# Kernel optimization log

Measured on AMD Instinct MI355X. Metric: run time of the kernel, lower is better.

Reference implementation:

```python
import jax, jax.numpy as jnp
import numpy as np

N = 20000   # nodes
E = 320000  # edges
G = 64      # graphs in batch
IN = 256    # in_dim
H = 256     # hidden_dim1
C = 2       # n_classes


def setup_inputs() -> dict:
    key = jax.random.key(0)
    ks = jax.random.split(key, 12)
    h = jax.random.normal(ks[0], (N, IN), jnp.float32)
    src = jax.random.randint(ks[1], (E,), 0, N)
    dst = jax.random.randint(ks[2], (E,), 0, N)
    graph_id = jnp.sort(jax.random.randint(ks[3], (N,), 0, G))
    s_in = 1.0 / np.sqrt(IN)
    s_h = 1.0 / np.sqrt(H)
    W_conv = jax.random.normal(ks[4], (IN, H), jnp.float32) * s_in
    b_conv = jnp.zeros((H,), jnp.float32)
    w_gate = jax.random.normal(ks[5], (H, 1), jnp.float32) * s_h
    b_gate = jnp.zeros((1,), jnp.float32)
    W1 = jax.random.normal(ks[6], (H, H), jnp.float32) * s_h
    b1 = jnp.zeros((H,), jnp.float32)
    W2 = jax.random.normal(ks[7], (H, C), jnp.float32) * s_h
    b2 = jnp.zeros((C,), jnp.float32)
    return dict(h=h, src=src, dst=dst, graph_id=graph_id, W_conv=W_conv,
                b_conv=b_conv, w_gate=w_gate, b_gate=b_gate, W1=W1, b1=b1,
                W2=W2, b2=b2)


def reference(h, src, dst, graph_id, W_conv, b_conv, w_gate, b_gate, W1, b1, W2, b2):
    ones_e = jnp.ones((E,), jnp.float32)
    # DGL GraphConv, norm='both': D_out^-1/2 on source, D_in^-1/2 on dest
    deg_out = jax.ops.segment_sum(ones_e, src, num_segments=N)
    deg_in = jax.ops.segment_sum(ones_e, dst, num_segments=N)
    hn = h * jax.lax.rsqrt(jnp.maximum(deg_out, 1.0))[:, None]
    hn = hn @ W_conv                       # [N, H] (weight applied before aggregation)
    agg = jax.ops.segment_sum(hn[src], dst, num_segments=N)  # gather + scatter-add
    agg = agg * jax.lax.rsqrt(jnp.maximum(deg_in, 1.0))[:, None] + b_conv
    hr = jax.nn.relu(agg)                  # F.relu after conv1
    # GlobalAttentionPooling: per-graph segment softmax over gate scores
    gate = hr @ w_gate + b_gate            # [N, 1]
    gmax = jax.ops.segment_max(gate, graph_id, num_segments=G)
    e = jnp.exp(gate - gmax[graph_id])
    denom = jax.ops.segment_sum(e, graph_id, num_segments=G)
    att = e / denom[graph_id]              # [N, 1] attention weights (g2)
    hg = jax.ops.segment_sum(att * hr, graph_id, num_segments=G)  # [G, H]
    # classifier heads (dropout is identity at inference)
    a2 = hg @ W1 + b1
    a3 = a2 @ W2 + b2
    return jax.nn.sigmoid(a3), att, hg
```

## Files before the change

### kernel.cpp

```cpp
#include <hip/hip_runtime.h>
#include <hip/hip_bf16.h>
#include <hip/hip_fp16.h>
#include <math.h>

#define NN 20000
#define EE 320000
#define GG 64
#define IND 256
#define HD 256
#define CC 2

typedef __hip_bfloat16 bf16;
typedef __attribute__((ext_vector_type(8))) short short8;
typedef __attribute__((ext_vector_type(4))) float f32x4;

__device__ __forceinline__ float b2f(bf16 x){ return __bfloat162float(x); }
__device__ __forceinline__ float bits2f(unsigned short b){
    union{ float f; unsigned u; } v; v.u = ((unsigned)b) << 16; return v.f;
}
__device__ __forceinline__ short f2bs(float x){
    union{ bf16 b; short s; } u; u.b = __float2bfloat16(x); return u.s;
}
__device__ __forceinline__ float ldf3(const void* p, size_t i, int c){
    if (c == 1) return b2f(((const bf16*)p)[i]);
    if (c == 2) return __half2float(((const __half*)p)[i]);
    return ((const float*)p)[i];
}
__device__ __forceinline__ int idec(const void* p, int i, int c){
    if (c == 1) return (int)(((const long long*)p)[i]);
    if (c == 2) return (int)(((const float*)p)[i]);
    if (c == 3) return (int)__half2float(((const __half*)p)[i]);
    return ((const int*)p)[i];
}

__global__ void k_detect(const void* src, const void* dst, const void* gid,
                         const unsigned short* h, const unsigned short* Wc,
                         const unsigned short* wg, const unsigned short* W1,
                         const unsigned short* W2, const unsigned short* bc,
                         int* icode, int* dcode){
    int blk = blockIdx.x;
    if (blk < 3){
        if (threadIdx.x != 0) return;
        const void* buf = (blk == 0) ? src : (blk == 1) ? dst : gid;
        int n     = (blk == 2) ? NN : EE;
        int bound = (blk == 2) ? GG : NN;
        int ok64 = 1, ok32 = 1, okf32 = 1, okf16 = 1;
        const long long* p64 = (const long long*)buf;
        for (int i = 0; i < 64; i++){
            long long v = p64[n/8 + i];
            if (v < 0 || v >= (long long)bound) ok64 = 0;
        }
        const int* p32 = (const int*)buf;
        const unsigned* pu = (const unsigned*)buf;
        for (int i = 0; i < 64; i++){
            int v = p32[n/4 + i];
            if (v < 0 || v >= bound) ok32 = 0;
            float f = __uint_as_float(pu[n/4 + i]);
            if (!(f >= 0.f && f < (float)bound)) okf32 = 0;
        }
        const __half* ph = (const __half*)buf;
        for (int i = 0; i < 64; i++){
            float f = __half2float(ph[n/2 + i]);
            if (!(f >= 0.f && f < (float)bound)) okf16 = 0;
        }
        icode[blk] = ok64 ? 1 : (ok32 ? 0 : (okf32 ? 2 : (okf16 ? 3 : 0)));
    } else {
        int t = threadIdx.x; if (t >= 6) return;
        const unsigned short* p = t==0?h:t==1?Wc:t==2?wg:t==3?W1:t==4?W2:bc;
        int cb = 0, cf = 0, nz = 0;
        for (int i = 0; i < 128; i += 2){
            unsigned u = p[i];
            nz += (u != 0);
            int e8 = (u >> 7) & 0xFF;
            int e5 = (u >> 10) & 0x1F;
            cb += (e8 >= 100 && e8 <= 141);
            cf += (e5 >= 4 && e5 <= 22);
        }
        dcode[t] = (nz < 8) ? 0 : (cb >= 60) ? 1 : ((cf >= 60) ? 2 : 0);
    }
}

__global__ void k_prep(const void* src_r, const void* dst_r, const void* gid_r,
                       const int* __restrict__ icode,
                       int* __restrict__ gid_i,
                       int* cnt_out, int* cnt_in){
    int i = blockIdx.x*256 + threadIdx.x;
    if (i < NN) gid_i[i] = idec(gid_r, i, icode[2]);
    if (i >= EE) return;
    int s = idec(src_r, i, icode[0]);
    int d = idec(dst_r, i, icode[1]);
    if ((unsigned)s < NN) atomicAdd(&cnt_out[s], 1);
    if ((unsigned)d < NN) atomicAdd(&cnt_in[d], 1);
}

__global__ __launch_bounds__(1024) void k_scan(const int* __restrict__ cnt_out,
                                               const int* __restrict__ cnt_in,
                                               const int* __restrict__ gid,
                                               float* rs_out, float* rs_in,
                                               int* __restrict__ row_start,
                                               int* gstart, int* gend){
    int t = threadIdx.x;
    for (int i = t; i < NN; i += 1024){
        rs_out[i] = rsqrtf(fmaxf((float)cnt_out[i], 1.f));
        rs_in[i]  = rsqrtf(fmaxf((float)cnt_in[i], 1.f));
    }
    __shared__ int part[1024];
    const int per = (NN + 1023)/1024;
    int lo = t*per, hi = min(lo+per, NN);
    int s = 0;
    for (int i = lo; i < hi; i++) s += cnt_in[i];
    part[t] = s; __syncthreads();
    for (int off = 1; off < 1024; off <<= 1){
        int v = (t >= off) ? part[t-off] : 0;
        __syncthreads();
        part[t] += v;
        __syncthreads();
    }
    int base = part[t] - s;
    for (int i = lo; i < hi; i++){ row_start[i] = base; base += cnt_in[i]; }
    if (t == 1023) row_start[NN] = part[1023];
    __shared__ int ls[GG+1];
    if (t <= GG){
        int a = 0, b = NN;
        while (a < b){
            int mid = (a + b) >> 1;
            if (gid[mid] < t) a = mid + 1; else b = mid;
        }
        ls[t] = a;
    }
    __syncthreads();
    if (t < GG){ gstart[t] = ls[t]; gend[t] = ls[t+1]; }
}

__global__ void k_fill(const void* src_r, const void* dst_r,
                       const int* __restrict__ icode,
                       const int* __restrict__ row_start, int* __restrict__ cursor,
                       int* __restrict__ csr_src){
    int e = blockIdx.x*256 + threadIdx.x;
    if (e >= EE) return;
    int s = idec(src_r, e, icode[0]);
    int d = idec(dst_r, e, icode[1]);
    if ((unsigned)s >= NN || (unsigned)d >= NN) return;
    int pos = atomicAdd(&cursor[d], 1);
    csr_src[row_start[d] + pos] = s;
}

__global__ void k_wprep(const void* __restrict__ W, const int* __restrict__ dcode,
                        bf16* __restrict__ Wb){
    int k = blockIdx.x;
    int n = threadIdx.x;
    Wb[(size_t)n*IND + k] = __float2bfloat16(ldf3(W, (size_t)k*HD + n, dcode[1]));
}

__global__ __launch_bounds__(256) void k_gemm1m(const void* __restrict__ h,
                                                const bf16* __restrict__ Wb,
                                                const float* __restrict__ rs_out,
                                                const int* __restrict__ dcode,
                                                bf16* __restrict__ hn){
    int fh = dcode[0];
    int tid = threadIdx.x;
    int wave = tid >> 6, lane = tid & 63;
    int q = lane >> 4, mr = lane & 15;
    int row0 = blockIdx.x * 32;
    int ncol0 = wave * 64;
    f32x4 acc[2][4] = {};
    const float* hf = (const float*)h;
    #pragma unroll
    for (int k0 = 0; k0 < IND; k0 += 32){
        short8 a[2], b[4];
        if (fh == 0){
            #pragma unroll
            for (int mi = 0; mi < 2; mi++){
                int r = row0 + mi*16 + mr;
                const float4* p = (const float4*)(hf + (size_t)r*IND + k0 + q*8);
                float4 v0 = p[0], v1 = p[1];
                a[mi][0] = f2bs(v0.x); a[mi][1] = f2bs(v0.y);
                a[mi][2] = f2bs(v0.z); a[mi][3] = f2bs(v0.w);
                a[mi][4] = f2bs(v1.x); a[mi][5] = f2bs(v1.y);
                a[mi][6] = f2bs(v1.z); a[mi][7] = f2bs(v1.w);
            }
        } else {
            #pragma unroll
            for (int mi = 0; mi < 2; mi++){
                int r = row0 + mi*16 + mr;
                #pragma unroll
                for (int j = 0; j < 8; j++)
                    a[mi][j] = f2bs(ldf3(h, (size_t)r*IND + k0 + q*8 + j, fh));
            }
        }
        #pragma unroll
        for (int ni = 0; ni < 4; ni++)
            b[ni] = *reinterpret_cast<const short8*>(
                        Wb + (size_t)(ncol0 + ni*16 + mr)*IND + k0 + q*8);
        #pragma unroll
        for (int mi = 0; mi < 2; mi++)
            #pragma unroll
            for (int ni = 0; ni < 4; ni++)
                acc[mi][ni] = __builtin_amdgcn_mfma_f32_16x16x32_bf16(
                                  a[mi], b[ni], acc[mi][ni], 0, 0, 0);
    }
    #pragma unroll
    for (int mi = 0; mi < 2; mi++){
        int rowb = row0 + mi*16 + q*4;
        #pragma unroll
        for (int r = 0; r < 4; r++){
            int row = rowb + r;
            float rs = rs_out[row];
            #pragma unroll
            for (int ni = 0; ni < 4; ni++)
                hn[(size_t)row*HD + ncol0 + ni*16 + mr] =
                    __float2bfloat16(acc[mi][ni][r] * rs);
        }
    }
}

__global__ __launch_bounds__(256) void k_gather(const bf16* __restrict__ hn,
                                                const float* __restrict__ rs_in,
                                                const int* __restrict__ row_start,
                                                const int* __restrict__ csr_src,
                                                const void* __restrict__ b_conv,
                                                const void* __restrict__ w_gate,
                                                const void* __restrict__ b_gate,
                                                const int* __restrict__ dcode,
                                                float* __restrict__ hr,
                                                float* __restrict__ gate){
    int wave = threadIdx.x >> 6, lane = threadIdx.x & 63;
    int n = blockIdx.x*4 + wave;
    if (n >= NN) return;
    int lo = row_start[n], hi = row_start[n+1];
    float ax = 0.f, ay = 0.f, az = 0.f, aw = 0.f;
    int j = lo;
    for (; j + 4 <= hi; j += 4){
        int s0 = csr_src[j], s1 = csr_src[j+1], s2 = csr_src[j+2], s3 = csr_src[j+3];
        ushort4 u0 = ((const ushort4*)(hn + (size_t)s0*HD))[lane];
        ushort4 u1 = ((const ushort4*)(hn + (size_t)s1*HD))[lane];
        ushort4 u2 = ((const ushort4*)(hn + (size_t)s2*HD))[lane];
        ushort4 u3 = ((const ushort4*)(hn + (size_t)s3*HD))[lane];
        ax += bits2f(u0.x) + bits2f(u1.x) + bits2f(u2.x) + bits2f(u3.x);
        ay += bits2f(u0.y) + bits2f(u1.y) + bits2f(u2.y) + bits2f(u3.y);
        az += bits2f(u0.z) + bits2f(u1.z) + bits2f(u2.z) + bits2f(u3.z);
        aw += bits2f(u0.w) + bits2f(u1.w) + bits2f(u2.w) + bits2f(u3.w);
    }
    for (; j < hi; j++){
        int s = csr_src[j];
        ushort4 u = ((const ushort4*)(hn + (size_t)s*HD))[lane];
        ax += bits2f(u.x); ay += bits2f(u.y); az += bits2f(u.z); aw += bits2f(u.w);
    }
    int db = dcode[5], fg = dcode[2];
    float rsn = rs_in[n];
    int c = lane*4;
    ax = fmaxf(fmaf(ax, rsn, ldf3(b_conv, c+0, db)), 0.f);
    ay = fmaxf(fmaf(ay, rsn, ldf3(b_conv, c+1, db)), 0.f);
    az = fmaxf(fmaf(az, rsn, ldf3(b_conv, c+2, db)), 0.f);
    aw = fmaxf(fmaf(aw, rsn, ldf3(b_conv, c+3, db)), 0.f);
    float4 v; v.x = ax; v.y = ay; v.z = az; v.w = aw;
    ((float4*)(hr + (size_t)n*HD))[lane] = v;
    float g = ax*ldf3(w_gate, c+0, fg) + ay*ldf3(w_gate, c+1, fg)
            + az*ldf3(w_gate, c+2, fg) + aw*ldf3(w_gate, c+3, fg);
    #pragma unroll
    for (int off = 32; off; off >>= 1) g += __shfl_down(g, off);
    if (lane == 0) gate[n] = g + ldf3(b_gate, 0, db);
}

__global__ __launch_bounds__(256) void k_soft(const int* __restrict__ gstart,
                                              const int* __restrict__ gend,
                                              float* __restrict__ gate,
                                              float* __restrict__ out_att){
    int g = blockIdx.x, t = threadIdx.x;
    int lo = gstart[g], hi = gend[g];
    if (lo >= hi) return;
    __shared__ float sm[256];
    float m = -INFINITY;
    for (int n = lo + t; n < hi; n += 256) m = fmaxf(m, gate[n]);
    sm[t] = m; __syncthreads();
    for (int s = 128; s; s >>= 1){ if (t < s) sm[t] = fmaxf(sm[t], sm[t+s]); __syncthreads(); }
    m = sm[0]; __syncthreads();
    float acc = 0.f;
    for (int n = lo + t; n < hi; n += 256){
        float e = expf(gate[n] - m);
        gate[n] = e;
        acc += e;
    }
    sm[t] = acc; __syncthreads();
    for (int s = 128; s; s >>= 1){ if (t < s) sm[t] += sm[t+s]; __syncthreads(); }
    float inv = 1.f / sm[0];
    for (int n = lo + t; n < hi; n += 256){
        float a = gate[n] * inv;
        gate[n] = a;
        out_att[n] = a;
    }
}

__global__ __launch_bounds__(256) void k_hg(const float* __restrict__ att,
                                            const float* __restrict__ hr,
                                            const int* __restrict__ gstart,
                                            const int* __restrict__ gend,
                                            float* __restrict__ hg){
    int g = blockIdx.x >> 3, part = blockIdx.x & 7;
    int c = threadIdx.x;
    int s = gstart[g], en = gend[g];
    int len = en - s;
    if (len <= 0) return;
    int chunk = (len + 7) >> 3;
    int lo = s + part*chunk, hi = min(lo + chunk, en);
    if (lo >= hi) return;
    float acc = 0.f;
    for (int n = lo; n < hi; n++) acc += att[n] * hr[(size_t)n*HD + c];
    atomicAdd(&hg[g*HD + c], acc);
}

__global__ __launch_bounds__(256) void k_cls(const float* __restrict__ hg,
                                             const void* __restrict__ W1,
                                             const void* __restrict__ b1,
                                             const void* __restrict__ W2,
                                             const void* __restrict__ b2,
                                             const int* __restrict__ dcode,
                                             float* __restrict__ out0,
                                             float* __restrict__ out_hg){
    int f1 = dcode[3], f2 = dcode[4], db = dcode[5];
    int g = blockIdx.x, tid = threadIdx.x;
    __shared__ float hs[256];
    float hv = hg[g*HD + tid];
    hs[tid] = hv;
    out_hg[g*HD + tid] = hv;
    __syncthreads();
    float acc = ldf3(b1, tid, db);
    if (f1 == 1){
        const bf16* w = (const bf16*)W1;
        for (int k = 0; k < HD; k++) acc += hs[k]*b2f(w[(size_t)k*HD + tid]);
    } else if (f1 == 2){
        const __half* w = (const __half*)W1;
        for (int k = 0; k < HD; k++) acc += hs[k]*__half2float(w[(size_t)k*HD + tid]);
    } else {
        const float* w = (const float*)W1;
        for (int k = 0; k < HD; k++) acc += hs[k]*w[(size_t)k*HD + tid];
    }
    float p0 = acc * ldf3(W2, tid*CC + 0, f2);
    float p1 = acc * ldf3(W2, tid*CC + 1, f2);
    __shared__ float r0[256], r1[256];
    r0[tid] = p0; r1[tid] = p1; __syncthreads();
    for (int s = 128; s; s >>= 1){
        if (tid < s){ r0[tid] += r0[tid+s]; r1[tid] += r1[tid+s]; }
        __syncthreads();
    }
    if (tid == 0){
        out0[g*CC+0] = 1.f/(1.f + expf(-(r0[0] + ldf3(b2, 0, db))));
        out0[g*CC+1] = 1.f/(1.f + expf(-(r1[0] + ldf3(b2, 1, db))));
    }
}

extern "C" void kernel_launch(void* const* d_in, const int* in_sizes, int n_in,
                              void* d_out, int out_size, void* d_ws, size_t ws_size,
                              hipStream_t stream) {
    const void* h      = d_in[0];
    const void* src_r  = d_in[1];
    const void* dst_r  = d_in[2];
    const void* gid_r  = d_in[3];
    const void* W_conv = d_in[4];
    const void* b_conv = d_in[5];
    const void* w_gate = d_in[6];
    const void* b_gate = d_in[7];
    const void* W1     = d_in[8];
    const void* b1     = d_in[9];
    const void* W2     = d_in[10];
    const void* b2     = d_in[11];

    float* out     = (float*)d_out;
    float* out0    = out;
    float* out_att = out + GG*CC;
    float* out_hg  = out + GG*CC + NN;

    char* w = (char*)d_ws;
    float* hr   = (float*)w;  w += (size_t)NN*HD*sizeof(float);
    bf16*  hn   = (bf16*)w;   w += (size_t)NN*HD*sizeof(bf16);
    bf16*  Wb   = (bf16*)w;   w += (size_t)IND*HD*sizeof(bf16);
    float* rs_o = (float*)w;  w += (size_t)NN*sizeof(float);
    float* rs_i = (float*)w;  w += (size_t)NN*sizeof(float);
    float* gate = (float*)w;  w += (size_t)NN*sizeof(float);
    float* hg   = (float*)w;  w += (size_t)GG*HD*sizeof(float);
    int* gstart = (int*)w;    w += GG*sizeof(int);
    int* gend   = (int*)w;    w += GG*sizeof(int);
    int* dcode  = (int*)w;    w += 8*sizeof(int);
    int* icode  = (int*)w;    w += 8*sizeof(int);
    int* gid_i  = (int*)w;    w += (size_t)NN*sizeof(int);
    int* cnt_out= (int*)w;    w += (size_t)NN*sizeof(int);
    int* cnt_in = (int*)w;    w += (size_t)NN*sizeof(int);
    int* cursor = (int*)w;    w += (size_t)NN*sizeof(int);
    int* rowst  = (int*)w;    w += (size_t)(NN+1)*sizeof(int);
    int* csr    = (int*)w;    w += (size_t)EE*sizeof(int);

    k_detect<<<4, 64, 0, stream>>>(src_r, dst_r, gid_r,
                                   (const unsigned short*)h, (const unsigned short*)W_conv,
                                   (const unsigned short*)w_gate, (const unsigned short*)W1,
                                   (const unsigned short*)W2, (const unsigned short*)b_conv,
                                   icode, dcode);

    hipMemsetAsync(hg, 0, (size_t)GG*HD*sizeof(float), stream);
    hipMemsetAsync(cnt_out, 0, (size_t)3*NN*sizeof(int), stream);

    k_prep<<<(EE+255)/256, 256, 0, stream>>>(src_r, dst_r, gid_r, icode,
                                             gid_i, cnt_out, cnt_in);
    k_scan<<<1, 1024, 0, stream>>>(cnt_out, cnt_in, gid_i, rs_o, rs_i,
                                   rowst, gstart, gend);
    k_fill<<<(EE+255)/256, 256, 0, stream>>>(src_r, dst_r, icode, rowst, cursor, csr);

    k_wprep<<<IND, HD, 0, stream>>>(W_conv, dcode, Wb);
    k_gemm1m<<<NN/32, 256, 0, stream>>>(h, Wb, rs_o, dcode, hn);

    k_gather<<<(NN+3)/4, 256, 0, stream>>>(hn, rs_i, rowst, csr,
                                           b_conv, w_gate, b_gate, dcode, hr, gate);

    k_soft<<<GG, 256, 0, stream>>>(gstart, gend, gate, out_att);
    k_hg<<<GG*8, 256, 0, stream>>>(gate, hr, gstart, gend, hg);
    k_cls<<<GG, 256, 0, stream>>>(hg, W1, b1, W2, b2, dcode, out0, out_hg);
}
```

Before: 257.3 us.

## Fuse softmax, pooling and classifier into one tail kernel; fold memsets into detect

```diff
diff --git a/kernel.cpp b/kernel.cpp
--- a/kernel.cpp
+++ b/kernel.cpp
@@ -33,12 +33,18 @@
     return ((const int*)p)[i];
 }
 
-__global__ void k_detect(const void* src, const void* dst, const void* gid,
+__global__ __launch_bounds__(256) void k_detect(const void* src, const void* dst,
+                         const void* gid,
                          const unsigned short* h, const unsigned short* Wc,
                          const unsigned short* wg, const unsigned short* W1,
                          const unsigned short* W2, const unsigned short* bc,
-                         int* icode, int* dcode){
+                         int* icode, int* dcode, int* zero_base){
     int blk = blockIdx.x;
+    if (blk >= 4){
+        int idx = (blk-4)*256 + threadIdx.x;
+        for (int i = idx; i < 3*NN; i += 60*256) zero_base[i] = 0;
+        return;
+    }
     if (blk < 3){
         if (threadIdx.x != 0) return;
         const void* buf = (blk == 0) ? src : (blk == 1) ? dst : gid;
@@ -230,16 +236,25 @@
     int lo = row_start[n], hi = row_start[n+1];
     float ax = 0.f, ay = 0.f, az = 0.f, aw = 0.f;
     int j = lo;
-    for (; j + 4 <= hi; j += 4){
-        int s0 = csr_src[j], s1 = csr_src[j+1], s2 = csr_src[j+2], s3 = csr_src[j+3];
+    for (; j + 8 <= hi; j += 8){
+        int s0 = csr_src[j+0], s1 = csr_src[j+1], s2 = csr_src[j+2], s3 = csr_src[j+3];
+        int s4 = csr_src[j+4], s5 = csr_src[j+5], s6 = csr_src[j+6], s7 = csr_src[j+7];
         ushort4 u0 = ((const ushort4*)(hn + (size_t)s0*HD))[lane];
         ushort4 u1 = ((const ushort4*)(hn + (size_t)s1*HD))[lane];
         ushort4 u2 = ((const ushort4*)(hn + (size_t)s2*HD))[lane];
         ushort4 u3 = ((const ushort4*)(hn + (size_t)s3*HD))[lane];
-        ax += bits2f(u0.x) + bits2f(u1.x) + bits2f(u2.x) + bits2f(u3.x);
-        ay += bits2f(u0.y) + bits2f(u1.y) + bits2f(u2.y) + bits2f(u3.y);
-        az += bits2f(u0.z) + bits2f(u1.z) + bits2f(u2.z) + bits2f(u3.z);
-        aw += bits2f(u0.w) + bits2f(u1.w) + bits2f(u2.w) + bits2f(u3.w);
+        ushort4 u4 = ((const ushort4*)(hn + (size_t)s4*HD))[lane];
+        ushort4 u5 = ((const ushort4*)(hn + (size_t)s5*HD))[lane];
+        ushort4 u6 = ((const ushort4*)(hn + (size_t)s6*HD))[lane];
+        ushort4 u7 = ((const ushort4*)(hn + (size_t)s7*HD))[lane];
+        ax += bits2f(u0.x)+bits2f(u1.x)+bits2f(u2.x)+bits2f(u3.x)
+            + bits2f(u4.x)+bits2f(u5.x)+bits2f(u6.x)+bits2f(u7.x);
+        ay += bits2f(u0.y)+bits2f(u1.y)+bits2f(u2.y)+bits2f(u3.y)
+            + bits2f(u4.y)+bits2f(u5.y)+bits2f(u6.y)+bits2f(u7.y);
+        az += bits2f(u0.z)+bits2f(u1.z)+bits2f(u2.z)+bits2f(u3.z)
+            + bits2f(u4.z)+bits2f(u5.z)+bits2f(u6.z)+bits2f(u7.z);
+        aw += bits2f(u0.w)+bits2f(u1.w)+bits2f(u2.w)+bits2f(u3.w)
+            + bits2f(u4.w)+bits2f(u5.w)+bits2f(u6.w)+bits2f(u7.w);
     }
     for (; j < hi; j++){
         int s = csr_src[j];
@@ -262,88 +277,78 @@
     if (lane == 0) gate[n] = g + ldf3(b_gate, 0, db);
 }
 
-__global__ __launch_bounds__(256) void k_soft(const int* __restrict__ gstart,
+__global__ __launch_bounds__(256) void k_tail(const int* __restrict__ gstart,
                                               const int* __restrict__ gend,
                                               float* __restrict__ gate,
-                                              float* __restrict__ out_att){
+                                              const float* __restrict__ hr,
+                                              const void* __restrict__ W1,
+                                              const void* __restrict__ b1,
+                                              const void* __restrict__ W2,
+                                              const void* __restrict__ b2,
+                                              const int* __restrict__ dcode,
+                                              float* __restrict__ out0,
+                                              float* __restrict__ out_att,
+                                              float* __restrict__ out_hg){
     int g = blockIdx.x, t = threadIdx.x;
     int lo = gstart[g], hi = gend[g];
-    if (lo >= hi) return;
     __shared__ float sm[256];
-    float m = -INFINITY;
-    for (int n = lo + t; n < hi; n += 256) m = fmaxf(m, gate[n]);
-    sm[t] = m; __syncthreads();
-    for (int s = 128; s; s >>= 1){ if (t < s) sm[t] = fmaxf(sm[t], sm[t+s]); __syncthreads(); }
-    m = sm[0]; __syncthreads();
+    __shared__ float hs[256];
+    if (lo < hi){
+        float m = -INFINITY;
+        for (int n = lo + t; n < hi; n += 256) m = fmaxf(m, gate[n]);
+        sm[t] = m; __syncthreads();
+        for (int s = 128; s; s >>= 1){ if (t < s) sm[t] = fmaxf(sm[t], sm[t+s]); __syncthreads(); }
+        m = sm[0]; __syncthreads();
+        float acc = 0.f;
+        for (int n = lo + t; n < hi; n += 256){
+            float e = expf(gate[n] - m);
+            gate[n] = e;
+            acc += e;
+        }
+        sm[t] = acc; __syncthreads();
+        for (int s = 128; s; s >>= 1){ if (t < s) sm[t] += sm[t+s]; __syncthreads(); }
+        float inv = 1.f / sm[0];
+        for (int n = lo + t; n < hi; n += 256){
+            float a = gate[n] * inv;
+            gate[n] = a;
+            out_att[n] = a;
+        }
+    }
+    __syncthreads();
     float acc = 0.f;
-    for (int n = lo + t; n < hi; n += 256){
-        float e = expf(gate[n] - m);
-        gate[n] = e;
-        acc += e;
-    }
-    sm[t] = acc; __syncthreads();
-    for (int s = 128; s; s >>= 1){ if (t < s) sm[t] += sm[t+s]; __syncthreads(); }
-    float inv = 1.f / sm[0];
-    for (int n = lo + t; n < hi; n += 256){
-        float a = gate[n] * inv;
-        gate[n] = a;
-        out_att[n] = a;
-    }
-}
-
-__global__ __launch_bounds__(256) void k_hg(const float* __restrict__ att,
-                                            const float* __restrict__ hr,
-                                            const int* __restrict__ gstart,
-                                            const int* __restrict__ gend,
-                                            float* __restrict__ hg){
-    int g = blockIdx.x >> 3, part = blockIdx.x & 7;
-    int c = threadIdx.x;
-    int s = gstart[g], en = gend[g];
-    int len = en - s;
-    if (len <= 0) return;
-    int chunk = (len + 7) >> 3;
-    int lo = s + part*chunk, hi = min(lo + chunk, en);
-    if (lo >= hi) return;
-    float acc = 0.f;
-    for (int n = lo; n < hi; n++) acc += att[n] * hr[(size_t)n*HD + c];
-    atomicAdd(&hg[g*HD + c], acc);
-}
-
-__global__ __launch_bounds__(256) void k_cls(const float* __restrict__ hg,
-                                             const void* __restrict__ W1,
-                                             const void* __restrict__ b1,
-                                             const void* __restrict__ W2,
-                                             const void* __restrict__ b2,
-                                             const int* __restrict__ dcode,
-                                             float* __restrict__ out0,
-                                             float* __restrict__ out_hg){
+    int n = lo;
+    for (; n + 4 <= hi; n += 4){
+        float a0 = gate[n], a1 = gate[n+1], a2 = gate[n+2], a3 = gate[n+3];
+        acc = fmaf(a0, hr[(size_t)n*HD + t], acc);
+        acc = fmaf(a1, hr[(size_t)(n+1)*HD + t], acc);
+        acc = fmaf(a2, hr[(size_t)(n+2)*HD + t], acc);
+        acc = fmaf(a3, hr[(size_t)(n+3)*HD + t], acc);
+    }
+    for (; n < hi; n++) acc = fmaf(gate[n], hr[(size_t)n*HD + t], acc);
+    hs[t] = acc;
+    out_hg[g*HD + t] = acc;
+    __syncthreads();
     int f1 = dcode[3], f2 = dcode[4], db = dcode[5];
-    int g = blockIdx.x, tid = threadIdx.x;
-    __shared__ float hs[256];
-    float hv = hg[g*HD + tid];
-    hs[tid] = hv;
-    out_hg[g*HD + tid] = hv;
-    __syncthreads();
-    float acc = ldf3(b1, tid, db);
+    float a2c = ldf3(b1, t, db);
     if (f1 == 1){
-        const bf16* w = (const bf16*)W1;
-        for (int k = 0; k < HD; k++) acc += hs[k]*b2f(w[(size_t)k*HD + tid]);
+        const bf16* wm = (const bf16*)W1;
+        for (int k = 0; k < HD; k++) a2c += hs[k]*b2f(wm[(size_t)k*HD + t]);
     } else if (f1 == 2){
-        const __half* w = (const __half*)W1;
-        for (int k = 0; k < HD; k++) acc += hs[k]*__half2float(w[(size_t)k*HD + tid]);
+        const __half* wm = (const __half*)W1;
+        for (int k = 0; k < HD; k++) a2c += hs[k]*__half2float(wm[(size_t)k*HD + t]);
     } else {
-        const float* w = (const float*)W1;
-        for (int k = 0; k < HD; k++) acc += hs[k]*w[(size_t)k*HD + tid];
-    }
-    float p0 = acc * ldf3(W2, tid*CC + 0, f2);
-    float p1 = acc * ldf3(W2, tid*CC + 1, f2);
+        const float* wm = (const float*)W1;
+        for (int k = 0; k < HD; k++) a2c += hs[k]*wm[(size_t)k*HD + t];
+    }
+    float p0 = a2c * ldf3(W2, t*CC + 0, f2);
+    float p1 = a2c * ldf3(W2, t*CC + 1, f2);
     __shared__ float r0[256], r1[256];
-    r0[tid] = p0; r1[tid] = p1; __syncthreads();
+    r0[t] = p0; r1[t] = p1; __syncthreads();
     for (int s = 128; s; s >>= 1){
-        if (tid < s){ r0[tid] += r0[tid+s]; r1[tid] += r1[tid+s]; }
+        if (t < s){ r0[t] += r0[t+s]; r1[t] += r1[t+s]; }
         __syncthreads();
     }
-    if (tid == 0){
+    if (t == 0){
         out0[g*CC+0] = 1.f/(1.f + expf(-(r0[0] + ldf3(b2, 0, db))));
         out0[g*CC+1] = 1.f/(1.f + expf(-(r1[0] + ldf3(b2, 1, db))));
     }
@@ -377,7 +382,6 @@
     float* rs_o = (float*)w;  w += (size_t)NN*sizeof(float);
     float* rs_i = (float*)w;  w += (size_t)NN*sizeof(float);
     float* gate = (float*)w;  w += (size_t)NN*sizeof(float);
-    float* hg   = (float*)w;  w += (size_t)GG*HD*sizeof(float);
     int* gstart = (int*)w;    w += GG*sizeof(int);
     int* gend   = (int*)w;    w += GG*sizeof(int);
     int* dcode  = (int*)w;    w += 8*sizeof(int);
@@ -389,14 +393,11 @@
     int* rowst  = (int*)w;    w += (size_t)(NN+1)*sizeof(int);
     int* csr    = (int*)w;    w += (size_t)EE*sizeof(int);
 
-    k_detect<<<4, 64, 0, stream>>>(src_r, dst_r, gid_r,
-                                   (const unsigned short*)h, (const unsigned short*)W_conv,
-                                   (const unsigned short*)w_gate, (const unsigned short*)W1,
-                                   (const unsigned short*)W2, (const unsigned short*)b_conv,
-                                   icode, dcode);
-
-    hipMemsetAsync(hg, 0, (size_t)GG*HD*sizeof(float), stream);
-    hipMemsetAsync(cnt_out, 0, (size_t)3*NN*sizeof(int), stream);
+    k_detect<<<64, 256, 0, stream>>>(src_r, dst_r, gid_r,
+                                     (const unsigned short*)h, (const unsigned short*)W_conv,
+                                     (const unsigned short*)w_gate, (const unsigned short*)W1,
+                                     (const unsigned short*)W2, (const unsigned short*)b_conv,
+                                     icode, dcode, cnt_out);
 
     k_prep<<<(EE+255)/256, 256, 0, stream>>>(src_r, dst_r, gid_r, icode,
                                              gid_i, cnt_out, cnt_in);
@@ -410,7 +411,6 @@
     k_gather<<<(NN+3)/4, 256, 0, stream>>>(hn, rs_i, rowst, csr,
                                            b_conv, w_gate, b_gate, dcode, hr, gate);
 
-    k_soft<<<GG, 256, 0, stream>>>(gstart, gend, gate, out_att);
-    k_hg<<<GG*8, 256, 0, stream>>>(gate, hr, gstart, gend, hg);
-    k_cls<<<GG, 256, 0, stream>>>(hg, W1, b1, W2, b2, dcode, out0, out_hg);
-}
+    k_tail<<<GG, 256, 0, stream>>>(gstart, gend, gate, hr,
+                                   W1, b1, W2, b2, dcode, out0, out_att, out_hg);
+}
```

Result: slower. 265.1 us (+3.0%).
